# Optimization experiments

Measured on AMD Instinct MI355X. Metric: run time of the kernel, lower is better.

## Reference

```python
import jax, jax.numpy as jnp
import numpy as np

B, S, E, U, V = 64, 1024, 1024, 1024, 32000

def setup_inputs() -> dict:
    key = jax.random.key(0)
    ks = jax.random.split(key, 12)
    s = lambda fan_in: 1.0 / np.sqrt(fan_in)
    return {
        "sentence": jax.random.randint(ks[0], (B, S), 0, V, dtype=jnp.int64),
        "emb": jax.random.normal(ks[1], (V, E), jnp.float32),
        "Wf": jax.random.normal(ks[2], (E, U), jnp.float32) * s(E),
        "bf": jnp.zeros((U,), jnp.float32),
        "Wi": jax.random.normal(ks[3], (E, U), jnp.float32) * s(E),
        "bi": jnp.zeros((U,), jnp.float32),
        "Wh": jax.random.normal(ks[4], (E, U), jnp.float32) * s(E),
        "bh": jnp.zeros((U,), jnp.float32),
        "W1": jax.random.normal(ks[5], (U, 64), jnp.float32) * s(U),
        "b1": jnp.zeros((64,), jnp.float32),
        "W2": jax.random.normal(ks[6], (64, 1), jnp.float32) * s(64),
        "b2": jnp.zeros((1,), jnp.float32),
    }

def reference(sentence, emb, Wf, bf, Wi, bi, Wh, bh, W1, b1, W2, b2):
    x = emb[sentence]                                   # [B,S,E]
    # minLSTM gates depend only on x -> hoist GEMMs out of the time loop
    f = jax.nn.sigmoid(jnp.einsum('bse,eu->bsu', x, Wf) + bf)
    i = jax.nn.sigmoid(jnp.einsum('bse,eu->bsu', x, Wi) + bi)
    h_tilde = jnp.einsum('bse,eu->bsu', x, Wh) + bh
    denom = f + i
    f_n = f / denom                                     # normalized forget gate
    i_n = i / denom                                     # normalized input gate

    def step(h, gates):
        f_t, ih_t = gates                               # [B,U] each
        h = f_t * h + ih_t
        return h, None

    h0 = jnp.zeros((sentence.shape[0], Wf.shape[1]), x.dtype)
    # scan over time; precombine i_n * h_tilde
    gates = (jnp.swapaxes(f_n, 0, 1), jnp.swapaxes(i_n * h_tilde, 0, 1))  # [S,B,U]
    h, _ = jax.lax.scan(step, h0, gates)
    z = h @ W1 + b1
    z = z @ W2 + b2
    return jax.nn.sigmoid(z)                            # [B,1]
```

## Files before the change

### kernel.cpp

```cpp
#include <hip/hip_runtime.h>
#include <cstdint>

typedef unsigned short u16;
typedef __attribute__((ext_vector_type(8))) short short8;
typedef __attribute__((ext_vector_type(8))) unsigned short ushort8;
typedef __attribute__((ext_vector_type(4))) float floatx4;
typedef __attribute__((ext_vector_type(8))) _Float16 half8;
typedef __attribute__((ext_vector_type(4))) unsigned uintx4;

#define S_LEN 1024
#define BATCH 64
#define EDIM 1024
#define UDIM 1024
#define VOCAB 32000
#define NTOT (3 * UDIM)
#define CT 64
#define NC (S_LEN / CT)

__device__ __forceinline__ u16 f2bf(float x) {
  unsigned u = __float_as_uint(x);
  return (u16)((u + 0x7fffu + ((u >> 16) & 1u)) >> 16);
}

__device__ __forceinline__ unsigned pk_bf16(float a, float b) {
  unsigned r;
  asm("v_cvt_pk_bf16_f32 %0, %1, %2" : "=v"(r) : "v"(a), "v"(b));
  return r;
}

__device__ __forceinline__ void async16(const u16* g, u16* s) {
  __builtin_amdgcn_global_load_lds(
      (__attribute__((address_space(1))) void*)(uintptr_t)g,
      (__attribute__((address_space(3))) void*)(uintptr_t)s,
      16, 0, 0);
}

__device__ __forceinline__ float sigm(float x) {
  return __builtin_amdgcn_rcpf(1.f + __expf(-x));
}

__global__ __launch_bounds__(256) void conv_wt(const float* __restrict__ Wf,
                                               const float* __restrict__ Wi,
                                               const float* __restrict__ Wh,
                                               u16* __restrict__ wtB) {
  __shared__ float t[32][33];
  const float* W = (blockIdx.z == 0) ? Wf : ((blockIdx.z == 1) ? Wi : Wh);
  int bx = blockIdx.x * 32;
  int by = blockIdx.y * 32;
  int tx = threadIdx.x, ty = threadIdx.y;
  for (int j = 0; j < 32; j += 8)
    t[ty + j][tx] = W[(size_t)(by + ty + j) * UDIM + bx + tx];
  __syncthreads();
  u16* out = wtB + (size_t)blockIdx.z * UDIM * EDIM;
  for (int j = 0; j < 32; j += 8)
    out[(size_t)(bx + ty + j) * EDIM + by + tx] = f2bf(t[tx][ty + j]);
}

__global__ __launch_bounds__(256, 3) void gate_gemm(
    const float* __restrict__ emb, const u16* __restrict__ wtB,
    const float* __restrict__ bfp, const float* __restrict__ bip,
    const float* __restrict__ bhp, u16* __restrict__ FG) {
  __shared__ __align__(16) u16 SM[128 * 64 + 192 * 64];
  u16* As = SM;
  u16* Bs = SM + 128 * 64;

  const int tid = threadIdx.x;
  const int wave = tid >> 6;
  const int lane = tid & 63;

  const int g = blockIdx.x;
  const int x = g & 7;
  const int s = g >> 3;
  const int mtile = s >> 1;
  const int utile = x * 2 + (s & 1);
  const int m0 = mtile * 128;
  const int u0 = utile * 64;

  const float* gAf[4]; int loA[4];
  const u16* gB[6]; int loB[6];
#pragma unroll
  for (int j = 0; j < 4; ++j) {
    int idx = j * 256 + tid;
    int r = idx >> 3;
    int cg = (idx & 7) ^ (r & 7);
    gAf[j] = emb + (size_t)(m0 + r) * EDIM + cg * 8;
    loA[j] = idx * 8;
  }
#pragma unroll
  for (int j = 0; j < 6; ++j) {
    int idx = j * 256 + tid;
    int r = idx >> 3;
    int gr = (r >> 6) * UDIM + u0 + (r & 63);
    int cg = (idx & 7) ^ (r & 7);
    gB[j] = wtB + (size_t)gr * EDIM + cg * 8;
    loB[j] = idx * 8;
  }

  floatx4 acc[8][3] = {};
  const int fr = lane & 15;
  const int fq = lane >> 4;
  const int fr7 = fr & 7;
  const int un = wave * 16 + fr;

  for (int k0 = 0; k0 < EDIM; k0 += 64) {
#pragma unroll
    for (int j = 0; j < 6; ++j) async16(gB[j] + k0, &Bs[loB[j]]);
    float4 fa[8];
#pragma unroll
    for (int j = 0; j < 4; ++j) {
      fa[2 * j] = *(const float4*)(gAf[j] + k0);
      fa[2 * j + 1] = *(const float4*)(gAf[j] + k0 + 4);
    }
#pragma unroll
    for (int j = 0; j < 4; ++j) {
      uintx4 p;
      p.x = pk_bf16(fa[2 * j].x, fa[2 * j].y);
      p.y = pk_bf16(fa[2 * j].z, fa[2 * j].w);
      p.z = pk_bf16(fa[2 * j + 1].x, fa[2 * j + 1].y);
      p.w = pk_bf16(fa[2 * j + 1].z, fa[2 * j + 1].w);
      *(short8*)&As[loA[j]] = __builtin_bit_cast(short8, p);
    }
    __syncthreads();
#pragma unroll
    for (int kk = 0; kk < 2; ++kk) {
      const int swz = ((kk * 4 + fq) ^ fr7) * 8;
      short8 b0 = *(const short8*)&Bs[(0 * 64 + un) * 64 + swz];
      short8 b1 = *(const short8*)&Bs[(1 * 64 + un) * 64 + swz];
      short8 b2 = *(const short8*)&Bs[(2 * 64 + un) * 64 + swz];
#pragma unroll
      for (int mt = 0; mt < 8; ++mt) {
        short8 am = *(const short8*)&As[(mt * 16 + fr) * 64 + swz];
        acc[mt][0] = __builtin_amdgcn_mfma_f32_16x16x32_bf16(am, b0, acc[mt][0], 0, 0, 0);
        acc[mt][1] = __builtin_amdgcn_mfma_f32_16x16x32_bf16(am, b1, acc[mt][1], 0, 0, 0);
        acc[mt][2] = __builtin_amdgcn_mfma_f32_16x16x32_bf16(am, b2, acc[mt][2], 0, 0, 0);
      }
    }
    __syncthreads();
  }

  const int ug = u0 + un;
  const float bfv = bfp[ug], biv = bip[ug], bhv = bhp[ug];
  u16* FGs = SM;
  const int up = un ^ ((fq & 1) << 4);
#pragma unroll
  for (int mt = 0; mt < 8; ++mt) {
#pragma unroll
    for (int r = 0; r < 4; ++r) {
      float fs = sigm(acc[mt][0][r] + bfv);
      float is = sigm(acc[mt][1][r] + biv);
      float hv = acc[mt][2][r] + bhv;
      float inv = __builtin_amdgcn_rcpf(fs + is);
      float fn = fs * inv;
      float gv = is * inv * hv;
      int row = mt * 16 + fq * 4 + r;
      unsigned pkfg = (unsigned)__builtin_bit_cast(u16, (_Float16)fn) |
                      ((unsigned)__builtin_bit_cast(u16, (_Float16)gv) << 16);
      *(unsigned*)&FGs[row * 128 + up * 2] = pkfg;
    }
  }
  __syncthreads();
#pragma unroll
  for (int j = 0; j < 8; ++j) {
    int idx = j * 256 + tid;
    int row = idx >> 4, cc = idx & 15;
    int ccp = cc ^ (((row >> 2) & 1) << 2);
    *(ushort8*)&FG[(size_t)(m0 + row) * (2 * UDIM) + u0 * 2 + cc * 8] =
        *(const ushort8*)&FGs[row * 128 + ccp * 8];
  }
}

__global__ __launch_bounds__(256) void scan_gather(
    const int* __restrict__ sent, const u16* __restrict__ FG,
    float* __restrict__ Fc, float* __restrict__ Gc) {
  const int b = blockIdx.x >> 4;
  const int c = blockIdx.x & (NC - 1);
  const int tid = threadIdx.x;
  __shared__ int toks[CT];
  if (tid < CT) toks[tid] = sent[b * S_LEN + c * CT + tid];
  __syncthreads();
  const int uo2 = tid * 8;
  floatx4 F = {1.f, 1.f, 1.f, 1.f};
  floatx4 G = {0.f, 0.f, 0.f, 0.f};
#pragma unroll 8
  for (int t = 0; t < CT; ++t) {
    const size_t ro = (size_t)toks[t] * (2 * UDIM) + uo2;
    half8 fg = __builtin_bit_cast(half8, *(const ushort8*)&FG[ro]);
    floatx4 fn = {(float)fg[0], (float)fg[2], (float)fg[4], (float)fg[6]};
    floatx4 gv = {(float)fg[1], (float)fg[3], (float)fg[5], (float)fg[7]};
    G = fn * G + gv;
    F = F * fn;
  }
  const size_t o = (size_t)c * (BATCH * UDIM) + (size_t)b * UDIM + tid * 4;
  *(floatx4*)&Fc[o] = F;
  *(floatx4*)&Gc[o] = G;
}

__global__ __launch_bounds__(256) void mlp_head(
    const float* __restrict__ Fc, const float* __restrict__ Gc,
    const float* __restrict__ W1, const float* __restrict__ b1,
    const float* __restrict__ W2, const float* __restrict__ b2,
    float* __restrict__ out) {
  const int b = blockIdx.x;
  const int tid = threadIdx.x;
  __shared__ float h_s[UDIM];
  __shared__ float z1[64];
  for (int u = tid; u < UDIM; u += 256) {
    float h = 0.f;
#pragma unroll
    for (int c = 0; c < NC; ++c) {
      float F = Fc[c * (BATCH * UDIM) + b * UDIM + u];
      float G = Gc[c * (BATCH * UDIM) + b * UDIM + u];
      h = F * h + G;
    }
    h_s[u] = h;
  }
  __syncthreads();
  const int j = tid >> 2, p = tid & 3;
  float partial = 0.f;
  for (int u = p * 256; u < p * 256 + 256; ++u) partial += h_s[u] * W1[u * 64 + j];
  partial += __shfl_down(partial, 1);
  partial += __shfl_down(partial, 2);
  if (p == 0) z1[j] = partial + b1[j];
  __syncthreads();
  if (tid < 64) {
    float v = z1[tid] * W2[tid];
#pragma unroll
    for (int off = 32; off > 0; off >>= 1) v += __shfl_down(v, off);
    if (tid == 0) out[b] = 1.f / (1.f + __expf(-(v + b2[0])));
  }
}

extern "C" void kernel_launch(void* const* d_in, const int* in_sizes, int n_in,
                              void* d_out, int out_size, void* d_ws, size_t ws_size,
                              hipStream_t stream) {
  const int* sent = (const int*)d_in[0];
  const float* emb = (const float*)d_in[1];
  const float* Wf = (const float*)d_in[2];
  const float* bf_ = (const float*)d_in[3];
  const float* Wi = (const float*)d_in[4];
  const float* bi_ = (const float*)d_in[5];
  const float* Wh = (const float*)d_in[6];
  const float* bh_ = (const float*)d_in[7];
  const float* W1 = (const float*)d_in[8];
  const float* b1 = (const float*)d_in[9];
  const float* W2 = (const float*)d_in[10];
  const float* b2 = (const float*)d_in[11];
  float* out = (float*)d_out;

  char* ws = (char*)d_ws;
  u16* wtB = (u16*)ws;    ws += (size_t)NTOT * EDIM * 2;
  u16* FG = (u16*)ws;     ws += (size_t)VOCAB * UDIM * 2 * 2;
  float* Fc = (float*)ws; ws += (size_t)NC * BATCH * UDIM * 4;
  float* Gc = (float*)ws; ws += (size_t)NC * BATCH * UDIM * 4;

  hipLaunchKernelGGL(conv_wt, dim3(32, 32, 3), dim3(32, 8), 0, stream, Wf, Wi, Wh, wtB);
  hipLaunchKernelGGL(gate_gemm, dim3((VOCAB / 128) * (NTOT / 192)), dim3(256), 0, stream,
                     emb, wtB, bf_, bi_, bh_, FG);
  hipLaunchKernelGGL(scan_gather, dim3(BATCH * NC), dim3(256), 0, stream,
                     sent, FG, Fc, Gc);
  hipLaunchKernelGGL(mlp_head, dim3(BATCH), dim3(256), 0, stream, Fc, Gc, W1, b1, W2, b2, out);
}
```

Before: 517.2 us.

## Pre-convert embedding to bf16 and double-buffer async LDS loads in gate GEMM

Adds a separate kernel that converts the whole fp32 embedding table to bf16 once, so the gate GEMM can load A tiles with async global-to-LDS copies instead of fp32 register loads plus conversion. The K loop becomes double-buffered: the next tile's A and B loads are issued before the MFMAs on the current buffer, with one wait and barrier per iteration. This is meant to hide load latency and halve A-side traffic inside the GEMM. The cost is an extra pass over the embedding table (read 128MB, write 64MB), doubled LDS use that lowers the occupancy target from 3 to 2 blocks, and a larger workspace.

```diff
diff --git a/kernel.cpp b/kernel.cpp
--- a/kernel.cpp
+++ b/kernel.cpp
@@ -6,7 +6,6 @@
 typedef __attribute__((ext_vector_type(8))) unsigned short ushort8;
 typedef __attribute__((ext_vector_type(4))) float floatx4;
 typedef __attribute__((ext_vector_type(8))) _Float16 half8;
-typedef __attribute__((ext_vector_type(4))) unsigned uintx4;
 
 #define S_LEN 1024
 #define BATCH 64
@@ -16,16 +15,11 @@
 #define NTOT (3 * UDIM)
 #define CT 64
 #define NC (S_LEN / CT)
+#define BUFE (128 * 64 + 192 * 64)
 
 __device__ __forceinline__ u16 f2bf(float x) {
   unsigned u = __float_as_uint(x);
   return (u16)((u + 0x7fffu + ((u >> 16) & 1u)) >> 16);
-}
-
-__device__ __forceinline__ unsigned pk_bf16(float a, float b) {
-  unsigned r;
-  asm("v_cvt_pk_bf16_f32 %0, %1, %2" : "=v"(r) : "v"(a), "v"(b));
-  return r;
 }
 
 __device__ __forceinline__ void async16(const u16* g, u16* s) {
@@ -37,6 +31,17 @@
 
 __device__ __forceinline__ float sigm(float x) {
   return __builtin_amdgcn_rcpf(1.f + __expf(-x));
+}
+
+__global__ __launch_bounds__(256) void conv_emb(const float4* __restrict__ in,
+                                                ushort4* __restrict__ out, int n4) {
+  const int stride = gridDim.x * 256;
+  for (int i = blockIdx.x * 256 + threadIdx.x; i < n4; i += stride) {
+    float4 v = in[i];
+    ushort4 o;
+    o.x = f2bf(v.x); o.y = f2bf(v.y); o.z = f2bf(v.z); o.w = f2bf(v.w);
+    out[i] = o;
+  }
 }
 
 __global__ __launch_bounds__(256) void conv_wt(const float* __restrict__ Wf,
@@ -56,13 +61,11 @@
     out[(size_t)(bx + ty + j) * EDIM + by + tx] = f2bf(t[tx][ty + j]);
 }
 
-__global__ __launch_bounds__(256, 3) void gate_gemm(
-    const float* __restrict__ emb, const u16* __restrict__ wtB,
+__global__ __launch_bounds__(256, 2) void gate_gemm(
+    const u16* __restrict__ embB, const u16* __restrict__ wtB,
     const float* __restrict__ bfp, const float* __restrict__ bip,
     const float* __restrict__ bhp, u16* __restrict__ FG) {
-  __shared__ __align__(16) u16 SM[128 * 64 + 192 * 64];
-  u16* As = SM;
-  u16* Bs = SM + 128 * 64;
+  __shared__ __align__(16) u16 SM[2 * BUFE];
 
   const int tid = threadIdx.x;
   const int wave = tid >> 6;
@@ -76,14 +79,14 @@
   const int m0 = mtile * 128;
   const int u0 = utile * 64;
 
-  const float* gAf[4]; int loA[4];
+  const u16* gA[4]; int loA[4];
   const u16* gB[6]; int loB[6];
 #pragma unroll
   for (int j = 0; j < 4; ++j) {
     int idx = j * 256 + tid;
     int r = idx >> 3;
     int cg = (idx & 7) ^ (r & 7);
-    gAf[j] = emb + (size_t)(m0 + r) * EDIM + cg * 8;
+    gA[j] = embB + (size_t)(m0 + r) * EDIM + cg * 8;
     loA[j] = idx * 8;
   }
 #pragma unroll
@@ -93,7 +96,7 @@
     int gr = (r >> 6) * UDIM + u0 + (r & 63);
     int cg = (idx & 7) ^ (r & 7);
     gB[j] = wtB + (size_t)gr * EDIM + cg * 8;
-    loB[j] = idx * 8;
+    loB[j] = 128 * 64 + idx * 8;
   }
 
   floatx4 acc[8][3] = {};
@@ -102,25 +105,27 @@
   const int fr7 = fr & 7;
   const int un = wave * 16 + fr;
 
-  for (int k0 = 0; k0 < EDIM; k0 += 64) {
-#pragma unroll
-    for (int j = 0; j < 6; ++j) async16(gB[j] + k0, &Bs[loB[j]]);
-    float4 fa[8];
-#pragma unroll
-    for (int j = 0; j < 4; ++j) {
-      fa[2 * j] = *(const float4*)(gAf[j] + k0);
-      fa[2 * j + 1] = *(const float4*)(gAf[j] + k0 + 4);
-    }
-#pragma unroll
-    for (int j = 0; j < 4; ++j) {
-      uintx4 p;
-      p.x = pk_bf16(fa[2 * j].x, fa[2 * j].y);
-      p.y = pk_bf16(fa[2 * j].z, fa[2 * j].w);
-      p.z = pk_bf16(fa[2 * j + 1].x, fa[2 * j + 1].y);
-      p.w = pk_bf16(fa[2 * j + 1].z, fa[2 * j + 1].w);
-      *(short8*)&As[loA[j]] = __builtin_bit_cast(short8, p);
-    }
-    __syncthreads();
+#pragma unroll
+  for (int j = 0; j < 4; ++j) async16(gA[j], &SM[loA[j]]);
+#pragma unroll
+  for (int j = 0; j < 6; ++j) async16(gB[j], &SM[loB[j]]);
+  asm volatile("s_waitcnt vmcnt(0)" ::: "memory");
+  __builtin_amdgcn_s_barrier();
+  __builtin_amdgcn_sched_barrier(0);
+
+  int cur = 0;
+  for (int t = 0; t < EDIM / 64; ++t) {
+    if (t + 1 < EDIM / 64) {
+      const int k0 = (t + 1) * 64;
+      u16* nb = SM + (cur ^ 1) * BUFE;
+#pragma unroll
+      for (int j = 0; j < 4; ++j) async16(gA[j] + k0, &nb[loA[j]]);
+#pragma unroll
+      for (int j = 0; j < 6; ++j) async16(gB[j] + k0, &nb[loB[j]]);
+    }
+    __builtin_amdgcn_sched_barrier(0);
+    const u16* As = SM + cur * BUFE;
+    const u16* Bs = As + 128 * 64;
 #pragma unroll
     for (int kk = 0; kk < 2; ++kk) {
       const int swz = ((kk * 4 + fq) ^ fr7) * 8;
@@ -135,7 +140,11 @@
         acc[mt][2] = __builtin_amdgcn_mfma_f32_16x16x32_bf16(am, b2, acc[mt][2], 0, 0, 0);
       }
     }
-    __syncthreads();
+    __builtin_amdgcn_sched_barrier(0);
+    asm volatile("s_waitcnt vmcnt(0)" ::: "memory");
+    __builtin_amdgcn_s_barrier();
+    __builtin_amdgcn_sched_barrier(0);
+    cur ^= 1;
   }
 
   const int ug = u0 + un;
@@ -248,14 +257,18 @@
   float* out = (float*)d_out;
 
   char* ws = (char*)d_ws;
+  u16* embB = (u16*)ws;   ws += (size_t)VOCAB * EDIM * 2;
   u16* wtB = (u16*)ws;    ws += (size_t)NTOT * EDIM * 2;
   u16* FG = (u16*)ws;     ws += (size_t)VOCAB * UDIM * 2 * 2;
   float* Fc = (float*)ws; ws += (size_t)NC * BATCH * UDIM * 4;
   float* Gc = (float*)ws; ws += (size_t)NC * BATCH * UDIM * 4;
 
+  int n4 = (int)((size_t)VOCAB * EDIM / 4);
+  hipLaunchKernelGGL(conv_emb, dim3(2048), dim3(256), 0, stream,
+                     (const float4*)emb, (ushort4*)embB, n4);
   hipLaunchKernelGGL(conv_wt, dim3(32, 32, 3), dim3(32, 8), 0, stream, Wf, Wi, Wh, wtB);
   hipLaunchKernelGGL(gate_gemm, dim3((VOCAB / 128) * (NTOT / 192)), dim3(256), 0, stream,
-                     emb, wtB, bf_, bi_, bh_, FG);
+                     embB, wtB, bf_, bi_, bh_, FG);
   hipLaunchKernelGGL(scan_gather, dim3(BATCH * NC), dim3(256), 0, stream,
                      sent, FG, Fc, Gc);
   hipLaunchKernelGGL(mlp_head, dim3(BATCH), dim3(256), 0, stream, Fc, Gc, W1, b1, W2, b2, out);
```

Measured after the change: 468.9 us. 9.3% less time.

## Pre-convert embedding table to bf16 and load GEMM A tiles asynchronously

Applied to the files above, without the earlier changes.

Adds a combined pre-pass kernel that transposes the gate weights and also converts the whole fp32 embedding table to bf16 in workspace. The gate GEMM then fetches A tiles with direct global-to-LDS async loads, like the B tiles, instead of loading fp32 into registers and packing to bf16 inside the K loop. This is meant to halve A-side traffic inside the GEMM and remove the register staging and conversion from its main loop. The cost is an extra full read of the fp32 table plus a bf16 write before the GEMM starts.

```diff
diff --git a/kernel.cpp b/kernel.cpp
--- a/kernel.cpp
+++ b/kernel.cpp
@@ -6,7 +6,6 @@
 typedef __attribute__((ext_vector_type(8))) unsigned short ushort8;
 typedef __attribute__((ext_vector_type(4))) float floatx4;
 typedef __attribute__((ext_vector_type(8))) _Float16 half8;
-typedef __attribute__((ext_vector_type(4))) unsigned uintx4;
 
 #define S_LEN 1024
 #define BATCH 64
@@ -16,16 +15,12 @@
 #define NTOT (3 * UDIM)
 #define CT 64
 #define NC (S_LEN / CT)
+#define NWT 3072
+#define NCE 2048
 
 __device__ __forceinline__ u16 f2bf(float x) {
   unsigned u = __float_as_uint(x);
   return (u16)((u + 0x7fffu + ((u >> 16) & 1u)) >> 16);
-}
-
-__device__ __forceinline__ unsigned pk_bf16(float a, float b) {
-  unsigned r;
-  asm("v_cvt_pk_bf16_f32 %0, %1, %2" : "=v"(r) : "v"(a), "v"(b));
-  return r;
 }
 
 __device__ __forceinline__ void async16(const u16* g, u16* s) {
@@ -39,25 +34,49 @@
   return __builtin_amdgcn_rcpf(1.f + __expf(-x));
 }
 
-__global__ __launch_bounds__(256) void conv_wt(const float* __restrict__ Wf,
-                                               const float* __restrict__ Wi,
-                                               const float* __restrict__ Wh,
-                                               u16* __restrict__ wtB) {
-  __shared__ float t[32][33];
-  const float* W = (blockIdx.z == 0) ? Wf : ((blockIdx.z == 1) ? Wi : Wh);
-  int bx = blockIdx.x * 32;
-  int by = blockIdx.y * 32;
-  int tx = threadIdx.x, ty = threadIdx.y;
-  for (int j = 0; j < 32; j += 8)
-    t[ty + j][tx] = W[(size_t)(by + ty + j) * UDIM + bx + tx];
-  __syncthreads();
-  u16* out = wtB + (size_t)blockIdx.z * UDIM * EDIM;
-  for (int j = 0; j < 32; j += 8)
-    out[(size_t)(bx + ty + j) * EDIM + by + tx] = f2bf(t[tx][ty + j]);
+__global__ __launch_bounds__(256) void conv_pre(
+    const float* __restrict__ Wf, const float* __restrict__ Wi,
+    const float* __restrict__ Wh, u16* __restrict__ wtB,
+    const float4* __restrict__ embIn, ushort4* __restrict__ embOut, int n4) {
+  const int b = blockIdx.x;
+  const int tid = threadIdx.x;
+  if (b < NWT) {
+    __shared__ float t[32][33];
+    const int z = b >> 10;
+    const int rem = b & 1023;
+    const int by = (rem >> 5) * 32;
+    const int bx = (rem & 31) * 32;
+    const float* W = (z == 0) ? Wf : ((z == 1) ? Wi : Wh);
+    const int tx = tid & 31, ty = tid >> 5;
+    for (int j = 0; j < 32; j += 8)
+      t[ty + j][tx] = W[(size_t)(by + ty + j) * UDIM + bx + tx];
+    __syncthreads();
+    u16* out = wtB + (size_t)z * UDIM * EDIM;
+    for (int j = 0; j < 32; j += 8)
+      out[(size_t)(bx + ty + j) * EDIM + by + tx] = f2bf(t[tx][ty + j]);
+  } else {
+    const int stride = NCE * 256;
+    int i = (b - NWT) * 256 + tid;
+    for (; i + stride < n4; i += 2 * stride) {
+      float4 v0 = embIn[i];
+      float4 v1 = embIn[i + stride];
+      ushort4 o0, o1;
+      o0.x = f2bf(v0.x); o0.y = f2bf(v0.y); o0.z = f2bf(v0.z); o0.w = f2bf(v0.w);
+      o1.x = f2bf(v1.x); o1.y = f2bf(v1.y); o1.z = f2bf(v1.z); o1.w = f2bf(v1.w);
+      embOut[i] = o0;
+      embOut[i + stride] = o1;
+    }
+    if (i < n4) {
+      float4 v = embIn[i];
+      ushort4 o;
+      o.x = f2bf(v.x); o.y = f2bf(v.y); o.z = f2bf(v.z); o.w = f2bf(v.w);
+      embOut[i] = o;
+    }
+  }
 }
 
 __global__ __launch_bounds__(256, 3) void gate_gemm(
-    const float* __restrict__ emb, const u16* __restrict__ wtB,
+    const u16* __restrict__ embB, const u16* __restrict__ wtB,
     const float* __restrict__ bfp, const float* __restrict__ bip,
     const float* __restrict__ bhp, u16* __restrict__ FG) {
   __shared__ __align__(16) u16 SM[128 * 64 + 192 * 64];
@@ -76,14 +95,14 @@
   const int m0 = mtile * 128;
   const int u0 = utile * 64;
 
-  const float* gAf[4]; int loA[4];
+  const u16* gA[4]; int loA[4];
   const u16* gB[6]; int loB[6];
 #pragma unroll
   for (int j = 0; j < 4; ++j) {
     int idx = j * 256 + tid;
     int r = idx >> 3;
     int cg = (idx & 7) ^ (r & 7);
-    gAf[j] = emb + (size_t)(m0 + r) * EDIM + cg * 8;
+    gA[j] = embB + (size_t)(m0 + r) * EDIM + cg * 8;
     loA[j] = idx * 8;
   }
 #pragma unroll
@@ -104,22 +123,9 @@
 
   for (int k0 = 0; k0 < EDIM; k0 += 64) {
 #pragma unroll
+    for (int j = 0; j < 4; ++j) async16(gA[j] + k0, &As[loA[j]]);
+#pragma unroll
     for (int j = 0; j < 6; ++j) async16(gB[j] + k0, &Bs[loB[j]]);
-    float4 fa[8];
-#pragma unroll
-    for (int j = 0; j < 4; ++j) {
-      fa[2 * j] = *(const float4*)(gAf[j] + k0);
-      fa[2 * j + 1] = *(const float4*)(gAf[j] + k0 + 4);
-    }
-#pragma unroll
-    for (int j = 0; j < 4; ++j) {
-      uintx4 p;
-      p.x = pk_bf16(fa[2 * j].x, fa[2 * j].y);
-      p.y = pk_bf16(fa[2 * j].z, fa[2 * j].w);
-      p.z = pk_bf16(fa[2 * j + 1].x, fa[2 * j + 1].y);
-      p.w = pk_bf16(fa[2 * j + 1].z, fa[2 * j + 1].w);
-      *(short8*)&As[loA[j]] = __builtin_bit_cast(short8, p);
-    }
     __syncthreads();
 #pragma unroll
     for (int kk = 0; kk < 2; ++kk) {
@@ -248,14 +254,17 @@
   float* out = (float*)d_out;
 
   char* ws = (char*)d_ws;
+  u16* embB = (u16*)ws;   ws += (size_t)VOCAB * EDIM * 2;
   u16* wtB = (u16*)ws;    ws += (size_t)NTOT * EDIM * 2;
   u16* FG = (u16*)ws;     ws += (size_t)VOCAB * UDIM * 2 * 2;
   float* Fc = (float*)ws; ws += (size_t)NC * BATCH * UDIM * 4;
   float* Gc = (float*)ws; ws += (size_t)NC * BATCH * UDIM * 4;
 
-  hipLaunchKernelGGL(conv_wt, dim3(32, 32, 3), dim3(32, 8), 0, stream, Wf, Wi, Wh, wtB);
+  int n4 = (int)((size_t)VOCAB * EDIM / 4);
+  hipLaunchKernelGGL(conv_pre, dim3(NWT + NCE), dim3(256), 0, stream,
+                     Wf, Wi, Wh, wtB, (const float4*)emb, (ushort4*)embB, n4);
   hipLaunchKernelGGL(gate_gemm, dim3((VOCAB / 128) * (NTOT / 192)), dim3(256), 0, stream,
-                     emb, wtB, bf_, bi_, bh_, FG);
+                     embB, wtB, bf_, bi_, bh_, FG);
   hipLaunchKernelGGL(scan_gather, dim3(BATCH * NC), dim3(256), 0, stream,
                      sent, FG, Fc, Gc);
   hipLaunchKernelGGL(mlp_head, dim3(BATCH), dim3(256), 0, stream, Fc, Gc, W1, b1, W2, b2, out);
```

Measured after the change: 470.2 us. 1.1x faster.
